# Performance work log

Hardware: AMD Instinct MI355X
Metric: run time of the kernel (lower is better)

The kernel has to match this reference:

```python
import jax, jax.numpy as jnp
import numpy as np

NUM_TIMESCALES = 16
MAX_TIME = 100.0
N_HEADS = 4
MLP_WIDTH = 128
HIDDEN_EACH = 128  # hidden_size // attn_n_heads = 512 // 4


def setup_inputs() -> dict:
    key = jax.random.key(0)
    ks = jax.random.split(key, 8)
    B, ROWS_PER_PAT, V = 32, 64, 32
    R = B * ROWS_PER_PAT
    # patient i has counts[i] observations, laid out row-major in its block of rows
    counts = 512 + 16 * np.arange(B)
    M = np.zeros((R, V), np.int32)
    for i in range(B):
        flat = M[i * ROWS_PER_PAT:(i + 1) * ROWS_PER_PAT].reshape(-1)
        flat[:counts[i]] = 1
    n_obs = int(counts.sum())        # 24320
    max_n_obs = int(counts.max())    # 1008
    n_in = 2 * NUM_TIMESCALES + 2    # 34

    def lin(k, o, i_):
        kw, kb = jax.random.split(k)
        return (jax.random.normal(kw, (o, i_)) * (1.0 / np.sqrt(i_)),
                jax.random.normal(kb, (o,)) * 0.01)

    W0, b0 = lin(ks[0], MLP_WIDTH, n_in)
    W1, b1 = lin(ks[1], MLP_WIDTH, MLP_WIDTH)
    W2, b2 = lin(ks[2], HIDDEN_EACH, MLP_WIDTH)
    Wq, bq = lin(ks[3], HIDDEN_EACH, HIDDEN_EACH)
    Wk, bk = lin(ks[4], HIDDEN_EACH, HIDDEN_EACH)
    return {
        "times": jax.random.uniform(ks[5], (R,)) * MAX_TIME,
        "time_ptr": jnp.arange(R + 1),
        "X": jax.random.normal(ks[6], (R, V)),
        "M": jnp.asarray(M),
        "obs_idx": jnp.repeat(jnp.arange(B), ROWS_PER_PAT),
        "pat_idx": jnp.arange(B),
        "W0": W0, "b0": b0, "W1": W1, "b1": b1, "W2": W2, "b2": b2,
        "Wq": Wq, "bq": bq, "Wk": Wk, "bk": bk,
        "n_obs": n_obs, "max_n_obs": max_n_obs,
    }


def reference(times, time_ptr, X, M, obs_idx, pat_idx,
              W0, b0, W1, b1, W2, b2, Wq, bq, Wk, bk, n_obs, max_n_obs):
    B = pat_idx.shape[0]
    # --- ragged scatter: (time_row, var) observations -> padded per-patient sets ---
    rows, cols = jnp.nonzero(M, size=n_obs)          # row-major, grouped by patient
    p = obs_idx[rows]                                # patient id per observation
    vals = X[rows, cols]
    t_arr = jnp.repeat(times, jnp.diff(time_ptr), total_repeat_length=X.shape[0])
    t = t_arr[rows]
    lens = jnp.bincount(p, length=B)
    starts = jnp.cumsum(lens) - lens
    pos = jnp.arange(n_obs) - starts[p]              # within-patient slot index
    Sv = jnp.zeros((B, max_n_obs), X.dtype).at[p, pos].set(cols.astype(X.dtype))
    Sx = jnp.zeros((B, max_n_obs), X.dtype).at[p, pos].set(vals)
    St = jnp.zeros((B, max_n_obs), X.dtype).at[p, pos].set(t)
    pad = jnp.arange(max_n_obs)[None, :] >= lens[:, None]   # True = padding
    # --- time embedding + feature concat: [sin, cos, var, value] ---
    timescales = MAX_TIME ** jnp.linspace(0.0, 1.0, NUM_TIMESCALES)
    st = St[..., None] / timescales
    new_X = jnp.concatenate([jnp.sin(st), jnp.cos(st), Sv[..., None], Sx[..., None]], axis=-1)
    # --- encoder MLP (depth 3 -> 1 hidden layer, eval mode: dropout is identity) ---
    h = jax.nn.relu(new_X @ W0.T + b0)
    h = jax.nn.relu(h @ W1.T + b1)
    enc = h @ W2.T + b2                              # [B, L, 128]
    # --- masked self-attention weights (only q/k matter; output is discarded) ---
    L = max_n_obs
    hd = HIDDEN_EACH // N_HEADS
    q = (enc @ Wq.T + bq).reshape(B, L, N_HEADS, hd)
    k = (enc @ Wk.T + bk).reshape(B, L, N_HEADS, hd)
    scores = jnp.einsum('blhd,bmhd->bhlm', q, k) / np.sqrt(hd)
    scores = jnp.where(pad[:, None, None, :], -1e30, scores)
    attn = jax.nn.softmax(scores, axis=-1)           # [B, H, L, L]
    w = attn[:, :, -1, :]                            # last-query attention row
    summed = jnp.einsum('bhl,ble->bhe', w, enc)      # [B, H, 128]
    return summed.reshape(B, -1)                     # [B, 512]
```

## Files before the change

### kernel.cpp

```cpp
#include <hip/hip_runtime.h>

#define B_PAT 32
#define RPP 64
#define RTOT 2048
#define NV 32
#define LMAX 1008
#define NTS 16
#define NIN 64
#define HW 128
#define LDSP 136
#define NCH 16
#define CH 63
#define ELD 132
#define RLD 136

typedef __attribute__((ext_vector_type(8))) short short8;
typedef __attribute__((ext_vector_type(4))) float floatx4;

__device__ __forceinline__ ushort f2b(float f) {
  unsigned int x = __float_as_uint(f);
  unsigned int r = (x + 0x7FFFu + ((x >> 16) & 1u)) >> 16;
  return (ushort)r;
}
__device__ __forceinline__ unsigned int pack2(ushort lo, ushort hi) {
  return (unsigned int)lo | ((unsigned int)hi << 16);
}
__device__ __forceinline__ unsigned long long shfl_up_u64(unsigned long long x, int off) {
  int lo = (int)(x & 0xffffffffull), hi = (int)(x >> 32);
  lo = __shfl_up(lo, off); hi = __shfl_up(hi, off);
  return ((unsigned long long)(unsigned int)hi << 32) | (unsigned long long)(unsigned int)lo;
}

__global__ __launch_bounds__(256) void k1_features(
    const float* __restrict__ times, const int* __restrict__ time_ptr,
    const float* __restrict__ X, const int* __restrict__ M,
    const int* __restrict__ obs_idx, const float* __restrict__ W0,
    const float* __restrict__ W1, const float* __restrict__ W2,
    ushort* __restrict__ feats, ushort* __restrict__ W0p,
    ushort* __restrict__ W1b, ushort* __restrict__ W2b, int* __restrict__ lens)
{
  const int b = blockIdx.x;
  const int t = threadIdx.x;
  if (b == B_PAT) {
    for (int i = t; i < HW * NIN; i += 256) {
      int n = i >> 6, k = i & 63;
      W0p[i] = (k < 34) ? f2b(W0[n * 34 + k]) : (ushort)0;
    }
    return;
  }
  if (b == B_PAT + 1) {
    for (int i = t; i < HW * HW; i += 256) W1b[i] = f2b(W1[i]);
    return;
  }
  if (b == B_PAT + 2) {
    for (int i = t; i < HW * HW; i += 256) W2b[i] = f2b(W2[i]);
    return;
  }
  __shared__ float inv_ts[NTS];
  __shared__ unsigned long long wsum[4];
  __shared__ int rowlist[RPP];
  __shared__ int rowpos[RPP];
  if (t < NTS) {
    float ts = powf(100.0f, (float)t * (1.0f / 15.0f));
    inv_ts[t] = 1.0f / ts;
  }
  const int lane = t & 63, wv = t >> 6;
  unsigned long long acc = 0ull;
  unsigned long long pref[8];
  const int rbase = t * 8;
#pragma unroll
  for (int j = 0; j < 8; ++j) {
    int r = rbase + j;
    int c = 0, pres = 0;
    if (obs_idx[r] == b) {
      pres = 1;
      const int4* mp = (const int4*)(M + r * NV);
#pragma unroll
      for (int q = 0; q < 8; ++q) {
        int4 m4 = mp[q];
        c += (m4.x != 0) + (m4.y != 0) + (m4.z != 0) + (m4.w != 0);
      }
    }
    pref[j] = acc;
    acc += (unsigned long long)(unsigned int)c | ((unsigned long long)pres << 32);
  }
  unsigned long long incl = acc;
  for (int off = 1; off < 64; off <<= 1) {
    unsigned long long v = shfl_up_u64(incl, off);
    if (lane >= off) incl += v;
  }
  if (lane == 63) wsum[wv] = incl;
  __syncthreads();
  unsigned long long wbase = 0ull;
  for (int w = 0; w < wv; ++w) wbase += wsum[w];
  unsigned long long totalall = wsum[0] + wsum[1] + wsum[2] + wsum[3];
  const int total = (int)(totalall & 0xffffffffull);
  const int nrows = (int)(totalall >> 32);
  unsigned long long myexcl = wbase + incl - acc;
#pragma unroll
  for (int j = 0; j < 8; ++j) {
    int r = rbase + j;
    if (obs_idx[r] == b) {
      unsigned long long p = myexcl + pref[j];
      int ord = (int)(p >> 32);
      if (ord < RPP) { rowlist[ord] = r; rowpos[ord] = (int)(p & 0xffffffffull); }
    }
  }
  if (t == 0) lens[b] = total;
  __syncthreads();
  const int o = t >> 2, sub = t & 3;
  if (o < nrows && o < RPP) {
    int r = rowlist[o];
    int base = rowpos[o];
    int lo = 0, hi = RTOT - 1;
    while (lo < hi) { int mid = (lo + hi + 1) >> 1; if (time_ptr[mid] <= r) lo = mid; else hi = mid - 1; }
    float tv = times[lo];
    float sv[NTS], cv[NTS];
#pragma unroll
    for (int i = 0; i < NTS; ++i) {
      float a = tv * inv_ts[i];
      sv[i] = sinf(a); cv[i] = cosf(a);
    }
    int cnt = 0;
    const int cb = sub * 8;
    for (int vv = 0; vv < cb; ++vv) cnt += (M[r * NV + vv] != 0);
    int pos = base + cnt;
    for (int vv = cb; vv < cb + 8; ++vv) {
      if (M[r * NV + vv] != 0) {
        unsigned int* fp = (unsigned int*)(feats + ((size_t)b * LMAX + pos) * NIN);
#pragma unroll
        for (int i = 0; i < 8; ++i) fp[i] = pack2(f2b(sv[2 * i]), f2b(sv[2 * i + 1]));
#pragma unroll
        for (int i = 0; i < 8; ++i) fp[8 + i] = pack2(f2b(cv[2 * i]), f2b(cv[2 * i + 1]));
        fp[16] = pack2(f2b((float)vv), f2b(X[r * NV + vv]));
#pragma unroll
        for (int i = 17; i < 32; ++i) fp[i] = 0u;
        ++pos;
      }
    }
  }
  {
    uint4 z = make_uint4(0u, 0u, 0u, 0u);
    uint4 one; one.x = one.y = one.z = one.w = 0x3F803F80u;
    for (int pos = total + t; pos < LMAX; pos += 256) {
      uint4* fp = (uint4*)(feats + ((size_t)b * LMAX + pos) * NIN);
      fp[0] = z; fp[1] = z; fp[2] = one; fp[3] = one;
      fp[4] = z; fp[5] = z; fp[6] = z; fp[7] = z;
    }
  }
}

__global__ __launch_bounds__(256) void k2_mlp(
    const ushort* __restrict__ feats, const ushort* __restrict__ W0p,
    const float* __restrict__ b0, const ushort* __restrict__ W1b,
    const float* __restrict__ b1, const ushort* __restrict__ W2b,
    const float* __restrict__ b2, float* __restrict__ enc)
{
  __shared__ ushort bufA[64 * LDSP];
  __shared__ ushort bufB[64 * LDSP];
  const int tid = threadIdx.x;
  const int wv = tid >> 6, lane = tid & 63;
  const int m16 = lane & 15, quad = lane >> 4;
  const int rowl = wv * 16 + m16;
  const size_t grow = (size_t)blockIdx.x * 64;
  {
    const short8* ar = (const short8*)(feats + (grow + rowl) * NIN);
    short8 a0 = ar[quad];
    short8 a1 = ar[4 + quad];
#pragma unroll
    for (int nt = 0; nt < 8; ++nt) {
      int n = nt * 16 + m16;
      const short8* br = (const short8*)(W0p + n * NIN);
      floatx4 acc = {0.f, 0.f, 0.f, 0.f};
      acc = __builtin_amdgcn_mfma_f32_16x16x32_bf16(a0, br[quad], acc, 0, 0, 0);
      acc = __builtin_amdgcn_mfma_f32_16x16x32_bf16(a1, br[4 + quad], acc, 0, 0, 0);
      float bias = b0[n];
#pragma unroll
      for (int i = 0; i < 4; ++i) {
        float vv = fmaxf(acc[i] + bias, 0.0f);
        bufA[(wv * 16 + quad * 4 + i) * LDSP + n] = f2b(vv);
      }
    }
  }
  __syncthreads();
  {
#pragma unroll
    for (int nt = 0; nt < 8; ++nt) {
      int n = nt * 16 + m16;
      floatx4 acc = {0.f, 0.f, 0.f, 0.f};
#pragma unroll
      for (int ks = 0; ks < 4; ++ks) {
        short8 a = *(const short8*)(bufA + rowl * LDSP + ks * 32 + quad * 8);
        short8 bb = *(const short8*)(W1b + n * HW + ks * 32 + quad * 8);
        acc = __builtin_amdgcn_mfma_f32_16x16x32_bf16(a, bb, acc, 0, 0, 0);
      }
      float bias = b1[n];
#pragma unroll
      for (int i = 0; i < 4; ++i) {
        float vv = fmaxf(acc[i] + bias, 0.0f);
        bufB[(wv * 16 + quad * 4 + i) * LDSP + n] = f2b(vv);
      }
    }
  }
  __syncthreads();
  {
#pragma unroll
    for (int nt = 0; nt < 8; ++nt) {
      int n = nt * 16 + m16;
      floatx4 acc = {0.f, 0.f, 0.f, 0.f};
#pragma unroll
      for (int ks = 0; ks < 4; ++ks) {
        short8 a = *(const short8*)(bufB + rowl * LDSP + ks * 32 + quad * 8);
        short8 bb = *(const short8*)(W2b + n * HW + ks * 32 + quad * 8);
        acc = __builtin_amdgcn_mfma_f32_16x16x32_bf16(a, bb, acc, 0, 0, 0);
      }
      float bias = b2[n];
#pragma unroll
      for (int i = 0; i < 4; ++i) {
        enc[(grow + wv * 16 + quad * 4 + i) * HW + n] = acc[i] + bias;
      }
    }
  }
}

__global__ __launch_bounds__(256) void k3_qr(
    const float* __restrict__ enc, const float* __restrict__ Wq,
    const float* __restrict__ bq, const float* __restrict__ Wk,
    float* __restrict__ r_all)
{
  const int b = blockIdx.x;
  const int tid = threadIdx.x;
  __shared__ float encq_s[HW], q_s[HW];
  const float* encb = enc + (size_t)b * LMAX * HW;
  if (tid < HW) encq_s[tid] = encb[(LMAX - 1) * HW + tid];
  __syncthreads();
  if (tid < HW) {
    float acc = bq[tid];
    const float4* wr = (const float4*)(Wq + tid * HW);
#pragma unroll 8
    for (int e4 = 0; e4 < 32; ++e4) {
      float4 w4 = wr[e4];
      acc += w4.x * encq_s[e4 * 4 + 0] + w4.y * encq_s[e4 * 4 + 1] +
             w4.z * encq_s[e4 * 4 + 2] + w4.w * encq_s[e4 * 4 + 3];
    }
    q_s[tid] = acc;
  }
  __syncthreads();
  const float scale = 0.17677669529663687f;
  for (int idx = tid; idx < 512; idx += 256) {
    int h = idx >> 7, e = idx & 127;
    float acc = 0.f;
#pragma unroll 8
    for (int d = 0; d < 32; ++d) acc += Wk[(h * 32 + d) * HW + e] * q_s[h * 32 + d];
    r_all[b * 512 + idx] = acc * scale;
  }
}

__global__ __launch_bounds__(256) void k3_chunk(
    const float* __restrict__ enc, const int* __restrict__ lens,
    const float* __restrict__ r_all, float* __restrict__ partial,
    float2* __restrict__ mxsm)
{
  const int bx = blockIdx.x;
  const int b = bx >> 4, c = bx & 15;
  const int tid = threadIdx.x;
  const int len = lens[b];
  const int start = c * CH;
  int valid = len - start; if (valid > CH) valid = CH;
  if (valid <= 0) {
    if (tid < 4) mxsm[bx * 4 + tid] = make_float2(-1e30f, 0.0f);
    return;
  }
  __shared__ float encs[CH * ELD];
  __shared__ float r_s[4 * RLD];
  __shared__ float lg[4 * 64];
  __shared__ float mx_s[4], sm_s[4];
  const float* encb = enc + ((size_t)b * LMAX + start) * HW;
  for (int i = tid; i < valid * 32; i += 256) {
    int row = i >> 5, e4 = i & 31;
    float4 v = ((const float4*)(encb + row * HW))[e4];
    *(float4*)(&encs[row * ELD + e4 * 4]) = v;
  }
  for (int i = tid; i < 512; i += 256)
    r_s[(i >> 7) * RLD + (i & 127)] = r_all[b * 512 + i];
  __syncthreads();
  {
    int m = tid >> 2, h = tid & 3;
    if (m < valid) {
      const float4* ev = (const float4*)(&encs[m * ELD]);
      const float4* rv = (const float4*)(&r_s[h * RLD]);
      float acc = 0.f;
#pragma unroll
      for (int e4 = 0; e4 < 32; ++e4) {
        float4 v = ev[e4], r = rv[e4];
        acc += v.x * r.x + v.y * r.y + v.z * r.z + v.w * r.w;
      }
      lg[h * 64 + m] = acc;
    }
  }
  __syncthreads();
  {
    const int wv = tid >> 6, lane = tid & 63;
    float v = (lane < valid) ? lg[wv * 64 + lane] : -1e30f;
    float mx = v;
#pragma unroll
    for (int o = 32; o >= 1; o >>= 1) mx = fmaxf(mx, __shfl_xor(mx, o));
    float p = (lane < valid) ? expf(v - mx) : 0.f;
    lg[wv * 64 + lane] = p;
    float sm = p;
#pragma unroll
    for (int o = 32; o >= 1; o >>= 1) sm += __shfl_xor(sm, o);
    if (lane == 0) { mx_s[wv] = mx; sm_s[wv] = sm; }
  }
  __syncthreads();
  for (int idx = tid; idx < 512; idx += 256) {
    int h = idx >> 7, e = idx & 127;
    float acc = 0.f;
    for (int m = 0; m < valid; ++m)
      acc += lg[h * 64 + m] * encs[m * ELD + e];
    partial[(size_t)bx * 512 + idx] = acc;
  }
  if (tid < 4) mxsm[bx * 4 + tid] = make_float2(mx_s[tid], sm_s[tid]);
}

__global__ __launch_bounds__(256) void k4_combine(
    const float* __restrict__ partial, const float2* __restrict__ mxsm,
    float* __restrict__ out)
{
  const int b = blockIdx.x;
  const int tid = threadIdx.x;
  __shared__ float f_s[NCH * 4];
  if (tid < 4) {
    int h = tid;
    float2 v[NCH];
    float M = -1e30f;
#pragma unroll
    for (int c = 0; c < NCH; ++c) {
      v[c] = mxsm[(b * NCH + c) * 4 + h];
      if (v[c].y > 0.f) M = fmaxf(M, v[c].x);
    }
    float S = 0.f;
#pragma unroll
    for (int c = 0; c < NCH; ++c)
      if (v[c].y > 0.f) S += v[c].y * expf(v[c].x - M);
    float invS = 1.0f / S;
#pragma unroll
    for (int c = 0; c < NCH; ++c)
      f_s[c * 4 + h] = (v[c].y > 0.f) ? expf(v[c].x - M) * invS : 0.f;
  }
  __syncthreads();
  for (int idx = tid; idx < 512; idx += 256) {
    int h = idx >> 7;
    float acc = 0.f;
#pragma unroll
    for (int c = 0; c < NCH; ++c)
      acc += partial[((size_t)(b * NCH + c)) * 512 + idx] * f_s[c * 4 + h];
    out[b * 512 + idx] = acc;
  }
}

extern "C" void kernel_launch(void* const* d_in, const int* in_sizes, int n_in,
                              void* d_out, int out_size, void* d_ws, size_t ws_size,
                              hipStream_t stream) {
  const float* times = (const float*)d_in[0];
  const int* time_ptr = (const int*)d_in[1];
  const float* X = (const float*)d_in[2];
  const int* M = (const int*)d_in[3];
  const int* obs_idx = (const int*)d_in[4];
  const float* W0 = (const float*)d_in[6];
  const float* b0 = (const float*)d_in[7];
  const float* W1 = (const float*)d_in[8];
  const float* b1 = (const float*)d_in[9];
  const float* W2 = (const float*)d_in[10];
  const float* b2 = (const float*)d_in[11];
  const float* Wq = (const float*)d_in[12];
  const float* bq = (const float*)d_in[13];
  const float* Wk = (const float*)d_in[14];
  float* out = (float*)d_out;

  char* ws = (char*)d_ws;
  size_t off = 0;
  ushort* feats = (ushort*)(ws + off); off += (size_t)B_PAT * LMAX * NIN * sizeof(ushort);
  ushort* W0p = (ushort*)(ws + off); off += (size_t)HW * NIN * sizeof(ushort);
  ushort* W1b = (ushort*)(ws + off); off += (size_t)HW * HW * sizeof(ushort);
  ushort* W2b = (ushort*)(ws + off); off += (size_t)HW * HW * sizeof(ushort);
  off = (off + 255) & ~(size_t)255;
  int* lens = (int*)(ws + off); off += 256;
  float* enc = (float*)(ws + off); off += (size_t)B_PAT * LMAX * HW * sizeof(float);
  float* r_all = (float*)(ws + off); off += (size_t)B_PAT * 512 * sizeof(float);
  float* partial = (float*)(ws + off); off += (size_t)B_PAT * NCH * 512 * sizeof(float);
  float2* mxsm = (float2*)(ws + off); off += (size_t)B_PAT * NCH * 4 * sizeof(float2);

  k1_features<<<B_PAT + 3, 256, 0, stream>>>(times, time_ptr, X, M, obs_idx,
                                             W0, W1, W2, feats, W0p, W1b, W2b, lens);
  k2_mlp<<<(B_PAT * LMAX) / 64, 256, 0, stream>>>(feats, W0p, b0, W1b, b1, W2b, b2, enc);
  k3_qr<<<B_PAT, 256, 0, stream>>>(enc, Wq, bq, Wk, r_all);
  k3_chunk<<<B_PAT * NCH, 256, 0, stream>>>(enc, lens, r_all, partial, mxsm);
  k4_combine<<<B_PAT, 256, 0, stream>>>(partial, mxsm, out);
}
```

Before: 157.7 us.

## Fuse encoder MLP into attention chunk kernel and compute query in feature kernel

Runs the three-layer encoder MLP inside the per-chunk attention kernel and keeps each chunk's encodings in shared memory, so the full fp32 enc tensor is never written to or read back from global memory. The last-row query projection is computed separately in the feature kernel with a scalar fp32 MLP, which removes the separate query kernel and one launch. Chunks past a patient's length now skip the MLP work entirely. In exchange the fused kernel uses much more shared memory per block, which can lower occupancy, and the serial query path adds latency to the feature kernel.

```diff
diff --git a/kernel.cpp b/kernel.cpp
--- a/kernel.cpp
+++ b/kernel.cpp
@@ -17,6 +17,9 @@
 typedef __attribute__((ext_vector_type(8))) short short8;
 typedef __attribute__((ext_vector_type(4))) float floatx4;
 
+__device__ __forceinline__ float b2f(ushort u) {
+  union { float f; unsigned int i; } v; v.i = ((unsigned int)u) << 16; return v.f;
+}
 __device__ __forceinline__ ushort f2b(float f) {
   unsigned int x = __float_as_uint(f);
   unsigned int r = (x + 0x7FFFu + ((x >> 16) & 1u)) >> 16;
@@ -35,9 +38,13 @@
     const float* __restrict__ times, const int* __restrict__ time_ptr,
     const float* __restrict__ X, const int* __restrict__ M,
     const int* __restrict__ obs_idx, const float* __restrict__ W0,
-    const float* __restrict__ W1, const float* __restrict__ W2,
+    const float* __restrict__ b0, const float* __restrict__ W1,
+    const float* __restrict__ b1, const float* __restrict__ W2,
+    const float* __restrict__ b2, const float* __restrict__ Wq,
+    const float* __restrict__ bq, const float* __restrict__ Wk,
     ushort* __restrict__ feats, ushort* __restrict__ W0p,
-    ushort* __restrict__ W1b, ushort* __restrict__ W2b, int* __restrict__ lens)
+    ushort* __restrict__ W1b, ushort* __restrict__ W2b,
+    int* __restrict__ lens, float* __restrict__ r_all)
 {
   const int b = blockIdx.x;
   const int t = threadIdx.x;
@@ -148,116 +155,67 @@
       fp[4] = z; fp[5] = z; fp[6] = z; fp[7] = z;
     }
   }
-}
-
-__global__ __launch_bounds__(256) void k2_mlp(
+  __syncthreads();
+  __shared__ float x_s[64];
+  __shared__ float h0_s[HW], h1_s[HW], eq_s[HW], q_s[HW];
+  __shared__ float part[256];
+  if (t < 64) x_s[t] = b2f(feats[((size_t)b * LMAX + (LMAX - 1)) * NIN + t]);
+  __syncthreads();
+  if (t < HW) {
+    float a2 = b0[t];
+#pragma unroll 2
+    for (int k = 0; k < 34; ++k) a2 += W0[t * 34 + k] * x_s[k];
+    h0_s[t] = fmaxf(a2, 0.0f);
+  }
+  __syncthreads();
+  {
+    int oo = t & 127, hf = t >> 7;
+    float a2 = 0.f;
+    const float* wr = W1 + oo * HW + hf * 64;
+#pragma unroll 8
+    for (int k = 0; k < 64; ++k) a2 += wr[k] * h0_s[hf * 64 + k];
+    part[t] = a2;
+  }
+  __syncthreads();
+  if (t < HW) h1_s[t] = fmaxf(part[t] + part[t + 128] + b1[t], 0.0f);
+  __syncthreads();
+  {
+    int oo = t & 127, hf = t >> 7;
+    float a2 = 0.f;
+    const float* wr = W2 + oo * HW + hf * 64;
+#pragma unroll 8
+    for (int k = 0; k < 64; ++k) a2 += wr[k] * h1_s[hf * 64 + k];
+    part[t] = a2;
+  }
+  __syncthreads();
+  if (t < HW) eq_s[t] = part[t] + part[t + 128] + b2[t];
+  __syncthreads();
+  {
+    int oo = t & 127, hf = t >> 7;
+    float a2 = 0.f;
+    const float* wr = Wq + oo * HW + hf * 64;
+#pragma unroll 8
+    for (int k = 0; k < 64; ++k) a2 += wr[k] * eq_s[hf * 64 + k];
+    part[t] = a2;
+  }
+  __syncthreads();
+  if (t < HW) q_s[t] = part[t] + part[t + 128] + bq[t];
+  __syncthreads();
+  const float scale = 0.17677669529663687f;
+  for (int idx = t; idx < 512; idx += 256) {
+    int h = idx >> 7, e = idx & 127;
+    float a2 = 0.f;
+#pragma unroll 8
+    for (int d = 0; d < 32; ++d) a2 += Wk[(h * 32 + d) * HW + e] * q_s[h * 32 + d];
+    r_all[b * 512 + idx] = a2 * scale;
+  }
+}
+
+__global__ __launch_bounds__(256) void k2_fused(
     const ushort* __restrict__ feats, const ushort* __restrict__ W0p,
     const float* __restrict__ b0, const ushort* __restrict__ W1b,
     const float* __restrict__ b1, const ushort* __restrict__ W2b,
-    const float* __restrict__ b2, float* __restrict__ enc)
-{
-  __shared__ ushort bufA[64 * LDSP];
-  __shared__ ushort bufB[64 * LDSP];
-  const int tid = threadIdx.x;
-  const int wv = tid >> 6, lane = tid & 63;
-  const int m16 = lane & 15, quad = lane >> 4;
-  const int rowl = wv * 16 + m16;
-  const size_t grow = (size_t)blockIdx.x * 64;
-  {
-    const short8* ar = (const short8*)(feats + (grow + rowl) * NIN);
-    short8 a0 = ar[quad];
-    short8 a1 = ar[4 + quad];
-#pragma unroll
-    for (int nt = 0; nt < 8; ++nt) {
-      int n = nt * 16 + m16;
-      const short8* br = (const short8*)(W0p + n * NIN);
-      floatx4 acc = {0.f, 0.f, 0.f, 0.f};
-      acc = __builtin_amdgcn_mfma_f32_16x16x32_bf16(a0, br[quad], acc, 0, 0, 0);
-      acc = __builtin_amdgcn_mfma_f32_16x16x32_bf16(a1, br[4 + quad], acc, 0, 0, 0);
-      float bias = b0[n];
-#pragma unroll
-      for (int i = 0; i < 4; ++i) {
-        float vv = fmaxf(acc[i] + bias, 0.0f);
-        bufA[(wv * 16 + quad * 4 + i) * LDSP + n] = f2b(vv);
-      }
-    }
-  }
-  __syncthreads();
-  {
-#pragma unroll
-    for (int nt = 0; nt < 8; ++nt) {
-      int n = nt * 16 + m16;
-      floatx4 acc = {0.f, 0.f, 0.f, 0.f};
-#pragma unroll
-      for (int ks = 0; ks < 4; ++ks) {
-        short8 a = *(const short8*)(bufA + rowl * LDSP + ks * 32 + quad * 8);
-        short8 bb = *(const short8*)(W1b + n * HW + ks * 32 + quad * 8);
-        acc = __builtin_amdgcn_mfma_f32_16x16x32_bf16(a, bb, acc, 0, 0, 0);
-      }
-      float bias = b1[n];
-#pragma unroll
-      for (int i = 0; i < 4; ++i) {
-        float vv = fmaxf(acc[i] + bias, 0.0f);
-        bufB[(wv * 16 + quad * 4 + i) * LDSP + n] = f2b(vv);
-      }
-    }
-  }
-  __syncthreads();
-  {
-#pragma unroll
-    for (int nt = 0; nt < 8; ++nt) {
-      int n = nt * 16 + m16;
-      floatx4 acc = {0.f, 0.f, 0.f, 0.f};
-#pragma unroll
-      for (int ks = 0; ks < 4; ++ks) {
-        short8 a = *(const short8*)(bufB + rowl * LDSP + ks * 32 + quad * 8);
-        short8 bb = *(const short8*)(W2b + n * HW + ks * 32 + quad * 8);
-        acc = __builtin_amdgcn_mfma_f32_16x16x32_bf16(a, bb, acc, 0, 0, 0);
-      }
-      float bias = b2[n];
-#pragma unroll
-      for (int i = 0; i < 4; ++i) {
-        enc[(grow + wv * 16 + quad * 4 + i) * HW + n] = acc[i] + bias;
-      }
-    }
-  }
-}
-
-__global__ __launch_bounds__(256) void k3_qr(
-    const float* __restrict__ enc, const float* __restrict__ Wq,
-    const float* __restrict__ bq, const float* __restrict__ Wk,
-    float* __restrict__ r_all)
-{
-  const int b = blockIdx.x;
-  const int tid = threadIdx.x;
-  __shared__ float encq_s[HW], q_s[HW];
-  const float* encb = enc + (size_t)b * LMAX * HW;
-  if (tid < HW) encq_s[tid] = encb[(LMAX - 1) * HW + tid];
-  __syncthreads();
-  if (tid < HW) {
-    float acc = bq[tid];
-    const float4* wr = (const float4*)(Wq + tid * HW);
-#pragma unroll 8
-    for (int e4 = 0; e4 < 32; ++e4) {
-      float4 w4 = wr[e4];
-      acc += w4.x * encq_s[e4 * 4 + 0] + w4.y * encq_s[e4 * 4 + 1] +
-             w4.z * encq_s[e4 * 4 + 2] + w4.w * encq_s[e4 * 4 + 3];
-    }
-    q_s[tid] = acc;
-  }
-  __syncthreads();
-  const float scale = 0.17677669529663687f;
-  for (int idx = tid; idx < 512; idx += 256) {
-    int h = idx >> 7, e = idx & 127;
-    float acc = 0.f;
-#pragma unroll 8
-    for (int d = 0; d < 32; ++d) acc += Wk[(h * 32 + d) * HW + e] * q_s[h * 32 + d];
-    r_all[b * 512 + idx] = acc * scale;
-  }
-}
-
-__global__ __launch_bounds__(256) void k3_chunk(
-    const float* __restrict__ enc, const int* __restrict__ lens,
+    const float* __restrict__ b2, const int* __restrict__ lens,
     const float* __restrict__ r_all, float* __restrict__ partial,
     float2* __restrict__ mxsm)
 {
@@ -269,38 +227,98 @@
   int valid = len - start; if (valid > CH) valid = CH;
   if (valid <= 0) {
     if (tid < 4) mxsm[bx * 4 + tid] = make_float2(-1e30f, 0.0f);
+    for (int i = tid; i < 512; i += 256) partial[(size_t)bx * 512 + i] = 0.f;
     return;
   }
+  __shared__ ushort bufA[64 * LDSP];
+  __shared__ ushort bufB[64 * LDSP];
   __shared__ float encs[CH * ELD];
   __shared__ float r_s[4 * RLD];
   __shared__ float lg[4 * 64];
   __shared__ float mx_s[4], sm_s[4];
-  const float* encb = enc + ((size_t)b * LMAX + start) * HW;
-  for (int i = tid; i < valid * 32; i += 256) {
-    int row = i >> 5, e4 = i & 31;
-    float4 v = ((const float4*)(encb + row * HW))[e4];
-    *(float4*)(&encs[row * ELD + e4 * 4]) = v;
-  }
+  const int wv = tid >> 6, lane = tid & 63;
+  const int m16 = lane & 15, quad = lane >> 4;
+  const int rowl = wv * 16 + m16;
+  const size_t fbase = (size_t)b * LMAX + start;
   for (int i = tid; i < 512; i += 256)
     r_s[(i >> 7) * RLD + (i & 127)] = r_all[b * 512 + i];
+  {
+    const int arow = (rowl < CH) ? rowl : (CH - 1);
+    const short8* ar = (const short8*)(feats + (fbase + arow) * NIN);
+    short8 a0 = ar[quad];
+    short8 a1 = ar[4 + quad];
+#pragma unroll
+    for (int nt = 0; nt < 8; ++nt) {
+      int n = nt * 16 + m16;
+      const short8* br = (const short8*)(W0p + n * NIN);
+      floatx4 acc2 = {0.f, 0.f, 0.f, 0.f};
+      acc2 = __builtin_amdgcn_mfma_f32_16x16x32_bf16(a0, br[quad], acc2, 0, 0, 0);
+      acc2 = __builtin_amdgcn_mfma_f32_16x16x32_bf16(a1, br[4 + quad], acc2, 0, 0, 0);
+      float bias = b0[n];
+#pragma unroll
+      for (int i = 0; i < 4; ++i) {
+        float vv = fmaxf(acc2[i] + bias, 0.0f);
+        bufA[(wv * 16 + quad * 4 + i) * LDSP + n] = f2b(vv);
+      }
+    }
+  }
+  __syncthreads();
+  {
+#pragma unroll
+    for (int nt = 0; nt < 8; ++nt) {
+      int n = nt * 16 + m16;
+      floatx4 acc2 = {0.f, 0.f, 0.f, 0.f};
+#pragma unroll
+      for (int ks = 0; ks < 4; ++ks) {
+        short8 a = *(const short8*)(bufA + rowl * LDSP + ks * 32 + quad * 8);
+        short8 bb = *(const short8*)(W1b + n * HW + ks * 32 + quad * 8);
+        acc2 = __builtin_amdgcn_mfma_f32_16x16x32_bf16(a, bb, acc2, 0, 0, 0);
+      }
+      float bias = b1[n];
+#pragma unroll
+      for (int i = 0; i < 4; ++i) {
+        float vv = fmaxf(acc2[i] + bias, 0.0f);
+        bufB[(wv * 16 + quad * 4 + i) * LDSP + n] = f2b(vv);
+      }
+    }
+  }
+  __syncthreads();
+  {
+#pragma unroll
+    for (int nt = 0; nt < 8; ++nt) {
+      int n = nt * 16 + m16;
+      floatx4 acc2 = {0.f, 0.f, 0.f, 0.f};
+#pragma unroll
+      for (int ks = 0; ks < 4; ++ks) {
+        short8 a = *(const short8*)(bufB + rowl * LDSP + ks * 32 + quad * 8);
+        short8 bb = *(const short8*)(W2b + n * HW + ks * 32 + quad * 8);
+        acc2 = __builtin_amdgcn_mfma_f32_16x16x32_bf16(a, bb, acc2, 0, 0, 0);
+      }
+      float bias = b2[n];
+#pragma unroll
+      for (int i = 0; i < 4; ++i) {
+        int orow = wv * 16 + quad * 4 + i;
+        if (orow < CH) encs[orow * ELD + n] = acc2[i] + bias;
+      }
+    }
+  }
   __syncthreads();
   {
     int m = tid >> 2, h = tid & 3;
     if (m < valid) {
       const float4* ev = (const float4*)(&encs[m * ELD]);
       const float4* rv = (const float4*)(&r_s[h * RLD]);
-      float acc = 0.f;
+      float acc2 = 0.f;
 #pragma unroll
       for (int e4 = 0; e4 < 32; ++e4) {
         float4 v = ev[e4], r = rv[e4];
-        acc += v.x * r.x + v.y * r.y + v.z * r.z + v.w * r.w;
-      }
-      lg[h * 64 + m] = acc;
-    }
-  }
-  __syncthreads();
-  {
-    const int wv = tid >> 6, lane = tid & 63;
+        acc2 += v.x * r.x + v.y * r.y + v.z * r.z + v.w * r.w;
+      }
+      lg[h * 64 + m] = acc2;
+    }
+  }
+  __syncthreads();
+  {
     float v = (lane < valid) ? lg[wv * 64 + lane] : -1e30f;
     float mx = v;
 #pragma unroll
@@ -315,10 +333,10 @@
   __syncthreads();
   for (int idx = tid; idx < 512; idx += 256) {
     int h = idx >> 7, e = idx & 127;
-    float acc = 0.f;
+    float acc2 = 0.f;
     for (int m = 0; m < valid; ++m)
-      acc += lg[h * 64 + m] * encs[m * ELD + e];
-    partial[(size_t)bx * 512 + idx] = acc;
+      acc2 += lg[h * 64 + m] * encs[m * ELD + e];
+    partial[(size_t)bx * 512 + idx] = acc2;
   }
   if (tid < 4) mxsm[bx * 4 + tid] = make_float2(mx_s[tid], sm_s[tid]);
 }
@@ -386,15 +404,14 @@
   ushort* W2b = (ushort*)(ws + off); off += (size_t)HW * HW * sizeof(ushort);
   off = (off + 255) & ~(size_t)255;
   int* lens = (int*)(ws + off); off += 256;
-  float* enc = (float*)(ws + off); off += (size_t)B_PAT * LMAX * HW * sizeof(float);
   float* r_all = (float*)(ws + off); off += (size_t)B_PAT * 512 * sizeof(float);
   float* partial = (float*)(ws + off); off += (size_t)B_PAT * NCH * 512 * sizeof(float);
   float2* mxsm = (float2*)(ws + off); off += (size_t)B_PAT * NCH * 4 * sizeof(float2);
 
   k1_features<<<B_PAT + 3, 256, 0, stream>>>(times, time_ptr, X, M, obs_idx,
-                                             W0, W1, W2, feats, W0p, W1b, W2b, lens);
-  k2_mlp<<<(B_PAT * LMAX) / 64, 256, 0, stream>>>(feats, W0p, b0, W1b, b1, W2b, b2, enc);
-  k3_qr<<<B_PAT, 256, 0, stream>>>(enc, Wq, bq, Wk, r_all);
-  k3_chunk<<<B_PAT * NCH, 256, 0, stream>>>(enc, lens, r_all, partial, mxsm);
+                                             W0, b0, W1, b1, W2, b2, Wq, bq, Wk,
+                                             feats, W0p, W1b, W2b, lens, r_all);
+  k2_fused<<<B_PAT * NCH, 256, 0, stream>>>(feats, W0p, b0, W1b, b1, W2b, b2,
+                                            lens, r_all, partial, mxsm);
   k4_combine<<<B_PAT, 256, 0, stream>>>(partial, mxsm, out);
 }
```

Result: faster. 151.9 us (-3.7%).

## Fuse feature build, MLP encoder and attention chunks into one per-row-pair kernel

Applied to the files above, without the earlier changes.

Restructures the pipeline so that each block takes two time rows of a patient, builds their feature tiles in LDS, runs the MLP with MFMA and immediately computes attention partials. The padded per-patient feature buffer and the full fp32 enc tensor in global memory are gone, and padding rows are no longer run through the MLP. The last-query row is recomputed separately in fp32 in a small kernel that produces q and r_all. This removes the large global round trips and the wasted padded work, at the cost of more kernels, more LDS per block and twice as many partial chunks to combine.

```diff
diff --git a/kernel.cpp b/kernel.cpp
--- a/kernel.cpp
+++ b/kernel.cpp
@@ -1,16 +1,15 @@
 #include <hip/hip_runtime.h>
 
 #define B_PAT 32
-#define RPP 64
 #define RTOT 2048
 #define NV 32
 #define LMAX 1008
 #define NTS 16
 #define NIN 64
+#define TLD 72
 #define HW 128
 #define LDSP 136
-#define NCH 16
-#define CH 63
+#define NCH2 32
 #define ELD 132
 #define RLD 136
 
@@ -25,146 +24,273 @@
 __device__ __forceinline__ unsigned int pack2(ushort lo, ushort hi) {
   return (unsigned int)lo | ((unsigned int)hi << 16);
 }
-__device__ __forceinline__ unsigned long long shfl_up_u64(unsigned long long x, int off) {
-  int lo = (int)(x & 0xffffffffull), hi = (int)(x >> 32);
-  lo = __shfl_up(lo, off); hi = __shfl_up(hi, off);
-  return ((unsigned long long)(unsigned int)hi << 32) | (unsigned long long)(unsigned int)lo;
-}
-
-__global__ __launch_bounds__(256) void k1_features(
+__device__ __forceinline__ float tscale(int i) {
+  return exp2f((float)i * (6.643856189774724f / 15.0f));
+}
+
+__global__ __launch_bounds__(256) void kA(
     const float* __restrict__ times, const int* __restrict__ time_ptr,
-    const float* __restrict__ X, const int* __restrict__ M,
-    const int* __restrict__ obs_idx, const float* __restrict__ W0,
+    const int* __restrict__ M, const float* __restrict__ W0,
     const float* __restrict__ W1, const float* __restrict__ W2,
-    ushort* __restrict__ feats, ushort* __restrict__ W0p,
-    ushort* __restrict__ W1b, ushort* __restrict__ W2b, int* __restrict__ lens)
+    int* __restrict__ row_cnt, float* __restrict__ trow,
+    ushort* __restrict__ W0p, ushort* __restrict__ W1b, ushort* __restrict__ W2b)
+{
+  const int blk = blockIdx.x, t = threadIdx.x;
+  if (blk >= 8) {
+    if (blk == 8) {
+      for (int i = t; i < HW * NIN; i += 256) {
+        int n = i >> 6, k = i & 63;
+        W0p[i] = (k < 34) ? f2b(W0[n * 34 + k]) : (ushort)0;
+      }
+    } else if (blk == 9) {
+      for (int i = t; i < HW * HW; i += 256) W1b[i] = f2b(W1[i]);
+    } else {
+      for (int i = t; i < HW * HW; i += 256) W2b[i] = f2b(W2[i]);
+    }
+    return;
+  }
+  const int r = blk * 256 + t;
+  const int4* mp = (const int4*)(M + r * NV);
+  int c = 0;
+#pragma unroll
+  for (int q = 0; q < 8; ++q) {
+    int4 m4 = mp[q];
+    c += (m4.x != 0) + (m4.y != 0) + (m4.z != 0) + (m4.w != 0);
+  }
+  row_cnt[r] = c;
+  int lo = 0, hi = RTOT - 1;
+  while (lo < hi) { int mid = (lo + hi + 1) >> 1; if (time_ptr[mid] <= r) lo = mid; else hi = mid - 1; }
+  trow[r] = times[lo];
+}
+
+__global__ __launch_bounds__(256) void kB(
+    const int* __restrict__ obs_idx, const int* __restrict__ row_cnt,
+    int* __restrict__ base, int* __restrict__ rowstart, int* __restrict__ lens)
+{
+  const int t = threadIdx.x;
+  const int lane = t & 63, wv = t >> 6;
+  __shared__ int wsum[4];
+  __shared__ int gpre[RTOT + 1];
+  __shared__ int rowstart_s[B_PAT + 1];
+  int cnt[8], pref[8];
+  int a = 0;
+  const int rbase = t * 8;
+#pragma unroll
+  for (int j = 0; j < 8; ++j) {
+    cnt[j] = row_cnt[rbase + j];
+    pref[j] = a; a += cnt[j];
+  }
+  int incl = a;
+  for (int off = 1; off < 64; off <<= 1) {
+    int v = __shfl_up(incl, off);
+    if (lane >= off) incl += v;
+  }
+  if (lane == 63) wsum[wv] = incl;
+  if (t == 0) rowstart_s[B_PAT] = RTOT;
+  __syncthreads();
+  int wbase = 0;
+  for (int w = 0; w < wv; ++w) wbase += wsum[w];
+  int excl = wbase + incl - a;
+#pragma unroll
+  for (int j = 0; j < 8; ++j) gpre[rbase + j] = excl + pref[j];
+  if (t == 255) gpre[RTOT] = excl + a;
+  for (int r = t; r < RTOT; r += 256) {
+    int b = obs_idx[r];
+    if (r == 0 || obs_idx[r - 1] != b) rowstart_s[b] = r;
+  }
+  __syncthreads();
+  if (t < B_PAT) {
+    int rs = rowstart_s[t], re = rowstart_s[t + 1];
+    lens[t] = gpre[re] - gpre[rs];
+    rowstart[t] = rs;
+  }
+  if (t == 0) rowstart[B_PAT] = RTOT;
+  for (int r = t; r < RTOT; r += 256)
+    base[r] = gpre[r] - gpre[rowstart_s[obs_idx[r]]];
+}
+
+__global__ __launch_bounds__(256) void kC(
+    const int* __restrict__ M, const float* __restrict__ X,
+    const float* __restrict__ trow, const int* __restrict__ base,
+    const int* __restrict__ row_cnt, const int* __restrict__ rowstart,
+    const int* __restrict__ lens,
+    const float* __restrict__ W0, const float* __restrict__ b0,
+    const float* __restrict__ W1, const float* __restrict__ b1,
+    const float* __restrict__ W2, const float* __restrict__ b2,
+    const float* __restrict__ Wq, const float* __restrict__ bq,
+    const float* __restrict__ Wk, float* __restrict__ r_all)
 {
   const int b = blockIdx.x;
   const int t = threadIdx.x;
-  if (b == B_PAT) {
-    for (int i = t; i < HW * NIN; i += 256) {
-      int n = i >> 6, k = i & 63;
-      W0p[i] = (k < 34) ? f2b(W0[n * 34 + k]) : (ushort)0;
-    }
+  __shared__ float x_s[64];
+  __shared__ float h0[HW], h1[HW], eq[HW], q_s[HW], part[256];
+  __shared__ int rc_s[2];
+  if (t < 64) x_s[t] = 0.0f;
+  if (t == 0) {
+    const int pos = LMAX - 1;
+    if (pos < lens[b]) {
+      int r = rowstart[b];
+      while (base[r] + row_cnt[r] <= pos) ++r;
+      int k = pos - base[r], c = 0;
+      for (int cc = 0; cc < NV; ++cc)
+        if (M[r * NV + cc] != 0) { if (k == 0) { c = cc; break; } --k; }
+      rc_s[0] = r; rc_s[1] = c;
+    } else rc_s[0] = -1;
+  }
+  __syncthreads();
+  if (rc_s[0] < 0) {
+    if (t >= 16 && t < 32) x_s[t] = 1.0f;
+  } else {
+    int r = rc_s[0], c = rc_s[1];
+    if (t < 16) {
+      float a = trow[r] / tscale(t);
+      x_s[t] = sinf(a); x_s[16 + t] = cosf(a);
+    }
+    if (t == 0) { x_s[32] = (float)c; x_s[33] = X[r * NV + c]; }
+  }
+  __syncthreads();
+  if (t < HW) {
+    float a = b0[t];
+#pragma unroll 2
+    for (int k = 0; k < 34; ++k) a += W0[t * 34 + k] * x_s[k];
+    h0[t] = fmaxf(a, 0.0f);
+  }
+  __syncthreads();
+  {
+    int oo = t & 127, hf = t >> 7;
+    float a = 0.f;
+    const float* wr = W1 + oo * HW + hf * 64;
+#pragma unroll 8
+    for (int k = 0; k < 64; ++k) a += wr[k] * h0[hf * 64 + k];
+    part[t] = a;
+  }
+  __syncthreads();
+  if (t < HW) h1[t] = fmaxf(part[t] + part[t + 128] + b1[t], 0.0f);
+  __syncthreads();
+  {
+    int oo = t & 127, hf = t >> 7;
+    float a = 0.f;
+    const float* wr = W2 + oo * HW + hf * 64;
+#pragma unroll 8
+    for (int k = 0; k < 64; ++k) a += wr[k] * h1[hf * 64 + k];
+    part[t] = a;
+  }
+  __syncthreads();
+  if (t < HW) eq[t] = part[t] + part[t + 128] + b2[t];
+  __syncthreads();
+  {
+    int oo = t & 127, hf = t >> 7;
+    float a = 0.f;
+    const float* wr = Wq + oo * HW + hf * 64;
+#pragma unroll 8
+    for (int k = 0; k < 64; ++k) a += wr[k] * eq[hf * 64 + k];
+    part[t] = a;
+  }
+  __syncthreads();
+  if (t < HW) q_s[t] = part[t] + part[t + 128] + bq[t];
+  __syncthreads();
+  const float scale = 0.17677669529663687f;
+  for (int idx = t; idx < 512; idx += 256) {
+    int h = idx >> 7, e = idx & 127;
+    float a = 0.f;
+#pragma unroll 8
+    for (int d = 0; d < 32; ++d) a += Wk[(h * 32 + d) * HW + e] * q_s[h * 32 + d];
+    r_all[b * 512 + idx] = a * scale;
+  }
+}
+
+__global__ __launch_bounds__(256) void kD(
+    const int* __restrict__ M, const float* __restrict__ X,
+    const float* __restrict__ trow, const int* __restrict__ base,
+    const int* __restrict__ row_cnt, const int* __restrict__ rowstart,
+    const ushort* __restrict__ W0p, const float* __restrict__ b0,
+    const ushort* __restrict__ W1b, const float* __restrict__ b1,
+    const ushort* __restrict__ W2b, const float* __restrict__ b2,
+    const float* __restrict__ r_all, float* __restrict__ partial,
+    float2* __restrict__ mxsm)
+{
+  const int bx = blockIdx.x;
+  const int b = bx >> 5, j = bx & 31;
+  const int t = threadIdx.x;
+  const int wv = t >> 6, lane = t & 63;
+  const int rs = rowstart[b], re = rowstart[b + 1];
+  const int r0 = rs + 2 * j;
+  if (r0 >= re) {
+    if (t < 4) mxsm[bx * 4 + t] = make_float2(-1e30f, 0.0f);
     return;
   }
-  if (b == B_PAT + 1) {
-    for (int i = t; i < HW * HW; i += 256) W1b[i] = f2b(W1[i]);
+  const int r1 = r0 + 1;
+  const bool has1 = (r1 < re);
+  const int pstart = base[r0];
+  const int valid = row_cnt[r0] + (has1 ? row_cnt[r1] : 0);
+  if (valid <= 0) {
+    if (t < 4) mxsm[bx * 4 + t] = make_float2(-1e30f, 0.0f);
     return;
   }
-  if (b == B_PAT + 2) {
-    for (int i = t; i < HW * HW; i += 256) W2b[i] = f2b(W2[i]);
-    return;
-  }
-  __shared__ float inv_ts[NTS];
-  __shared__ unsigned long long wsum[4];
-  __shared__ int rowlist[RPP];
-  __shared__ int rowpos[RPP];
-  if (t < NTS) {
-    float ts = powf(100.0f, (float)t * (1.0f / 15.0f));
-    inv_ts[t] = 1.0f / ts;
-  }
-  const int lane = t & 63, wv = t >> 6;
-  unsigned long long acc = 0ull;
-  unsigned long long pref[8];
-  const int rbase = t * 8;
-#pragma unroll
-  for (int j = 0; j < 8; ++j) {
-    int r = rbase + j;
-    int c = 0, pres = 0;
-    if (obs_idx[r] == b) {
-      pres = 1;
-      const int4* mp = (const int4*)(M + r * NV);
-#pragma unroll
-      for (int q = 0; q < 8; ++q) {
-        int4 m4 = mp[q];
-        c += (m4.x != 0) + (m4.y != 0) + (m4.z != 0) + (m4.w != 0);
-      }
-    }
-    pref[j] = acc;
-    acc += (unsigned long long)(unsigned int)c | ((unsigned long long)pres << 32);
-  }
-  unsigned long long incl = acc;
-  for (int off = 1; off < 64; off <<= 1) {
-    unsigned long long v = shfl_up_u64(incl, off);
-    if (lane >= off) incl += v;
-  }
-  if (lane == 63) wsum[wv] = incl;
-  __syncthreads();
-  unsigned long long wbase = 0ull;
-  for (int w = 0; w < wv; ++w) wbase += wsum[w];
-  unsigned long long totalall = wsum[0] + wsum[1] + wsum[2] + wsum[3];
-  const int total = (int)(totalall & 0xffffffffull);
-  const int nrows = (int)(totalall >> 32);
-  unsigned long long myexcl = wbase + incl - acc;
-#pragma unroll
-  for (int j = 0; j < 8; ++j) {
-    int r = rbase + j;
-    if (obs_idx[r] == b) {
-      unsigned long long p = myexcl + pref[j];
-      int ord = (int)(p >> 32);
-      if (ord < RPP) { rowlist[ord] = r; rowpos[ord] = (int)(p & 0xffffffffull); }
-    }
-  }
-  if (t == 0) lens[b] = total;
-  __syncthreads();
-  const int o = t >> 2, sub = t & 3;
-  if (o < nrows && o < RPP) {
-    int r = rowlist[o];
-    int base = rowpos[o];
-    int lo = 0, hi = RTOT - 1;
-    while (lo < hi) { int mid = (lo + hi + 1) >> 1; if (time_ptr[mid] <= r) lo = mid; else hi = mid - 1; }
-    float tv = times[lo];
-    float sv[NTS], cv[NTS];
-#pragma unroll
-    for (int i = 0; i < NTS; ++i) {
-      float a = tv * inv_ts[i];
-      sv[i] = sinf(a); cv[i] = cosf(a);
-    }
-    int cnt = 0;
-    const int cb = sub * 8;
-    for (int vv = 0; vv < cb; ++vv) cnt += (M[r * NV + vv] != 0);
-    int pos = base + cnt;
-    for (int vv = cb; vv < cb + 8; ++vv) {
-      if (M[r * NV + vv] != 0) {
-        unsigned int* fp = (unsigned int*)(feats + ((size_t)b * LMAX + pos) * NIN);
-#pragma unroll
-        for (int i = 0; i < 8; ++i) fp[i] = pack2(f2b(sv[2 * i]), f2b(sv[2 * i + 1]));
-#pragma unroll
-        for (int i = 0; i < 8; ++i) fp[8 + i] = pack2(f2b(cv[2 * i]), f2b(cv[2 * i + 1]));
-        fp[16] = pack2(f2b((float)vv), f2b(X[r * NV + vv]));
-#pragma unroll
-        for (int i = 17; i < 32; ++i) fp[i] = 0u;
-        ++pos;
-      }
-    }
-  }
+  __shared__ __align__(16) char arena[55296];
+  ushort* tile = (ushort*)(arena);
+  ushort* bufA = (ushort*)(arena + 9216);
+  float*  encs = (float*)(arena);
+  ushort* bufB = (ushort*)(arena + 33792);
+  float*  r_s  = (float*)(arena + 51200);
+  float*  lg   = (float*)(arena + 53376);
+  unsigned int* mapP = (unsigned int*)(arena + 54400);
+  unsigned int* mapT = (unsigned int*)(arena + 54656);
+  ushort* tps  = (ushort*)(arena + 54912);
+  float*  mx_s = (float*)(arena + 55040);
+  float*  sm_s = (float*)(arena + 55056);
   {
     uint4 z = make_uint4(0u, 0u, 0u, 0u);
-    uint4 one; one.x = one.y = one.z = one.w = 0x3F803F80u;
-    for (int pos = total + t; pos < LMAX; pos += 256) {
-      uint4* fp = (uint4*)(feats + ((size_t)b * LMAX + pos) * NIN);
-      fp[0] = z; fp[1] = z; fp[2] = one; fp[3] = one;
-      fp[4] = z; fp[5] = z; fp[6] = z; fp[7] = z;
-    }
-  }
-}
-
-__global__ __launch_bounds__(256) void k2_mlp(
-    const ushort* __restrict__ feats, const ushort* __restrict__ W0p,
-    const float* __restrict__ b0, const ushort* __restrict__ W1b,
-    const float* __restrict__ b1, const ushort* __restrict__ W2b,
-    const float* __restrict__ b2, float* __restrict__ enc)
-{
-  __shared__ ushort bufA[64 * LDSP];
-  __shared__ ushort bufB[64 * LDSP];
-  const int tid = threadIdx.x;
-  const int wv = tid >> 6, lane = tid & 63;
+    uint4* tp = (uint4*)tile;
+    for (int i = t; i < 576; i += 256) tp[i] = z;
+    for (int i = t; i < 512; i += 256)
+      r_s[(i >> 7) * RLD + (i & 127)] = r_all[b * 512 + i];
+  }
+  __syncthreads();
+  if (wv == 0) {
+    int rr = lane >> 5, cc = lane & 31;
+    int r = r0 + rr;
+    bool present = (rr == 0 || has1) ? (M[r * NV + cc] != 0) : false;
+    unsigned long long mask = __ballot(present);
+    unsigned int mh = (rr == 0) ? (unsigned int)mask : (unsigned int)(mask >> 32);
+    if (present) {
+      int rank = __popc(mh & ((1u << cc) - 1u));
+      int lp = base[r] - pstart + rank;
+      mapP[lp] = pack2(f2b((float)cc), f2b(X[r * NV + cc]));
+      mapT[lp] = (unsigned int)rr;
+    }
+  }
+  if (wv == 1 && lane < 32) {
+    int rr = lane >> 4, i = lane & 15;
+    if (rr == 0 || has1) {
+      float a = trow[r0 + rr] / tscale(i);
+      tps[rr * 32 + i] = f2b(sinf(a));
+      tps[rr * 32 + 16 + i] = f2b(cosf(a));
+    }
+  }
+  __syncthreads();
+  {
+    int lp = t >> 2, jj = t & 3;
+    if (lp < valid) {
+      int rr = (int)mapT[lp];
+      unsigned int* dst = (unsigned int*)(tile + lp * TLD);
+      const unsigned int* tp = ((const unsigned int*)tps) + rr * 16;
+      if (jj == 0) {
+#pragma unroll
+        for (int k = 0; k < 8; ++k) dst[k] = tp[k];
+      } else if (jj == 1) {
+#pragma unroll
+        for (int k = 0; k < 8; ++k) dst[8 + k] = tp[8 + k];
+      } else if (jj == 2) {
+        dst[16] = mapP[lp];
+      }
+    }
+  }
+  __syncthreads();
   const int m16 = lane & 15, quad = lane >> 4;
   const int rowl = wv * 16 + m16;
-  const size_t grow = (size_t)blockIdx.x * 64;
-  {
-    const short8* ar = (const short8*)(feats + (grow + rowl) * NIN);
+  {
+    const short8* ar = (const short8*)(tile + rowl * TLD);
     short8 a0 = ar[quad];
     short8 a1 = ar[4 + quad];
 #pragma unroll
@@ -216,76 +342,13 @@
       }
       float bias = b2[n];
 #pragma unroll
-      for (int i = 0; i < 4; ++i) {
-        enc[(grow + wv * 16 + quad * 4 + i) * HW + n] = acc[i] + bias;
-      }
-    }
-  }
-}
-
-__global__ __launch_bounds__(256) void k3_qr(
-    const float* __restrict__ enc, const float* __restrict__ Wq,
-    const float* __restrict__ bq, const float* __restrict__ Wk,
-    float* __restrict__ r_all)
-{
-  const int b = blockIdx.x;
-  const int tid = threadIdx.x;
-  __shared__ float encq_s[HW], q_s[HW];
-  const float* encb = enc + (size_t)b * LMAX * HW;
-  if (tid < HW) encq_s[tid] = encb[(LMAX - 1) * HW + tid];
-  __syncthreads();
-  if (tid < HW) {
-    float acc = bq[tid];
-    const float4* wr = (const float4*)(Wq + tid * HW);
-#pragma unroll 8
-    for (int e4 = 0; e4 < 32; ++e4) {
-      float4 w4 = wr[e4];
-      acc += w4.x * encq_s[e4 * 4 + 0] + w4.y * encq_s[e4 * 4 + 1] +
-             w4.z * encq_s[e4 * 4 + 2] + w4.w * encq_s[e4 * 4 + 3];
-    }
-    q_s[tid] = acc;
-  }
-  __syncthreads();
-  const float scale = 0.17677669529663687f;
-  for (int idx = tid; idx < 512; idx += 256) {
-    int h = idx >> 7, e = idx & 127;
-    float acc = 0.f;
-#pragma unroll 8
-    for (int d = 0; d < 32; ++d) acc += Wk[(h * 32 + d) * HW + e] * q_s[h * 32 + d];
-    r_all[b * 512 + idx] = acc * scale;
-  }
-}
-
-__global__ __launch_bounds__(256) void k3_chunk(
-    const float* __restrict__ enc, const int* __restrict__ lens,
-    const float* __restrict__ r_all, float* __restrict__ partial,
-    float2* __restrict__ mxsm)
-{
-  const int bx = blockIdx.x;
-  const int b = bx >> 4, c = bx & 15;
-  const int tid = threadIdx.x;
-  const int len = lens[b];
-  const int start = c * CH;
-  int valid = len - start; if (valid > CH) valid = CH;
-  if (valid <= 0) {
-    if (tid < 4) mxsm[bx * 4 + tid] = make_float2(-1e30f, 0.0f);
-    return;
-  }
-  __shared__ float encs[CH * ELD];
-  __shared__ float r_s[4 * RLD];
-  __shared__ float lg[4 * 64];
-  __shared__ float mx_s[4], sm_s[4];
-  const float* encb = enc + ((size_t)b * LMAX + start) * HW;
-  for (int i = tid; i < valid * 32; i += 256) {
-    int row = i >> 5, e4 = i & 31;
-    float4 v = ((const float4*)(encb + row * HW))[e4];
-    *(float4*)(&encs[row * ELD + e4 * 4]) = v;
-  }
-  for (int i = tid; i < 512; i += 256)
-    r_s[(i >> 7) * RLD + (i & 127)] = r_all[b * 512 + i];
-  __syncthreads();
-  {
-    int m = tid >> 2, h = tid & 3;
+      for (int i = 0; i < 4; ++i)
+        encs[(wv * 16 + quad * 4 + i) * ELD + n] = acc[i] + bias;
+    }
+  }
+  __syncthreads();
+  {
+    int m = t >> 2, h = t & 3;
     if (m < valid) {
       const float4* ev = (const float4*)(&encs[m * ELD]);
       const float4* rv = (const float4*)(&r_s[h * RLD]);
@@ -300,7 +363,6 @@
   }
   __syncthreads();
   {
-    const int wv = tid >> 6, lane = tid & 63;
     float v = (lane < valid) ? lg[wv * 64 + lane] : -1e30f;
     float mx = v;
 #pragma unroll
@@ -313,14 +375,14 @@
     if (lane == 0) { mx_s[wv] = mx; sm_s[wv] = sm; }
   }
   __syncthreads();
-  for (int idx = tid; idx < 512; idx += 256) {
+  for (int idx = t; idx < 512; idx += 256) {
     int h = idx >> 7, e = idx & 127;
     float acc = 0.f;
     for (int m = 0; m < valid; ++m)
       acc += lg[h * 64 + m] * encs[m * ELD + e];
     partial[(size_t)bx * 512 + idx] = acc;
   }
-  if (tid < 4) mxsm[bx * 4 + tid] = make_float2(mx_s[tid], sm_s[tid]);
+  if (t < 4) mxsm[bx * 4 + t] = make_float2(mx_s[t], sm_s[t]);
 }
 
 __global__ __launch_bounds__(256) void k4_combine(
@@ -329,23 +391,23 @@
 {
   const int b = blockIdx.x;
   const int tid = threadIdx.x;
-  __shared__ float f_s[NCH * 4];
+  __shared__ float f_s[NCH2 * 4];
   if (tid < 4) {
     int h = tid;
-    float2 v[NCH];
+    float2 v[NCH2];
     float M = -1e30f;
 #pragma unroll
-    for (int c = 0; c < NCH; ++c) {
-      v[c] = mxsm[(b * NCH + c) * 4 + h];
+    for (int c = 0; c < NCH2; ++c) {
+      v[c] = mxsm[(b * NCH2 + c) * 4 + h];
       if (v[c].y > 0.f) M = fmaxf(M, v[c].x);
     }
     float S = 0.f;
 #pragma unroll
-    for (int c = 0; c < NCH; ++c)
+    for (int c = 0; c < NCH2; ++c)
       if (v[c].y > 0.f) S += v[c].y * expf(v[c].x - M);
     float invS = 1.0f / S;
 #pragma unroll
-    for (int c = 0; c < NCH; ++c)
+    for (int c = 0; c < NCH2; ++c)
       f_s[c * 4 + h] = (v[c].y > 0.f) ? expf(v[c].x - M) * invS : 0.f;
   }
   __syncthreads();
@@ -353,8 +415,8 @@
     int h = idx >> 7;
     float acc = 0.f;
 #pragma unroll
-    for (int c = 0; c < NCH; ++c)
-      acc += partial[((size_t)(b * NCH + c)) * 512 + idx] * f_s[c * 4 + h];
+    for (int c = 0; c < NCH2; ++c)
+      acc += partial[((size_t)(b * NCH2 + c)) * 512 + idx] * f_s[c * 4 + h];
     out[b * 512 + idx] = acc;
   }
 }
@@ -380,21 +442,23 @@
 
   char* ws = (char*)d_ws;
   size_t off = 0;
-  ushort* feats = (ushort*)(ws + off); off += (size_t)B_PAT * LMAX * NIN * sizeof(ushort);
-  ushort* W0p = (ushort*)(ws + off); off += (size_t)HW * NIN * sizeof(ushort);
-  ushort* W1b = (ushort*)(ws + off); off += (size_t)HW * HW * sizeof(ushort);
-  ushort* W2b = (ushort*)(ws + off); off += (size_t)HW * HW * sizeof(ushort);
-  off = (off + 255) & ~(size_t)255;
+  int* row_cnt = (int*)(ws + off); off += RTOT * 4;
+  float* trow = (float*)(ws + off); off += RTOT * 4;
+  int* base = (int*)(ws + off); off += RTOT * 4;
+  int* rowstart = (int*)(ws + off); off += 256;
   int* lens = (int*)(ws + off); off += 256;
-  float* enc = (float*)(ws + off); off += (size_t)B_PAT * LMAX * HW * sizeof(float);
-  float* r_all = (float*)(ws + off); off += (size_t)B_PAT * 512 * sizeof(float);
-  float* partial = (float*)(ws + off); off += (size_t)B_PAT * NCH * 512 * sizeof(float);
-  float2* mxsm = (float2*)(ws + off); off += (size_t)B_PAT * NCH * 4 * sizeof(float2);
-
-  k1_features<<<B_PAT + 3, 256, 0, stream>>>(times, time_ptr, X, M, obs_idx,
-                                             W0, W1, W2, feats, W0p, W1b, W2b, lens);
-  k2_mlp<<<(B_PAT * LMAX) / 64, 256, 0, stream>>>(feats, W0p, b0, W1b, b1, W2b, b2, enc);
-  k3_qr<<<B_PAT, 256, 0, stream>>>(enc, Wq, bq, Wk, r_all);
-  k3_chunk<<<B_PAT * NCH, 256, 0, stream>>>(enc, lens, r_all, partial, mxsm);
+  ushort* W0p = (ushort*)(ws + off); off += (size_t)HW * NIN * 2;
+  ushort* W1b = (ushort*)(ws + off); off += (size_t)HW * HW * 2;
+  ushort* W2b = (ushort*)(ws + off); off += (size_t)HW * HW * 2;
+  float* r_all = (float*)(ws + off); off += (size_t)B_PAT * 512 * 4;
+  float* partial = (float*)(ws + off); off += (size_t)B_PAT * NCH2 * 512 * 4;
+  float2* mxsm = (float2*)(ws + off); off += (size_t)B_PAT * NCH2 * 4 * 8;
+
+  kA<<<11, 256, 0, stream>>>(times, time_ptr, M, W0, W1, W2, row_cnt, trow, W0p, W1b, W2b);
+  kB<<<1, 256, 0, stream>>>(obs_idx, row_cnt, base, rowstart, lens);
+  kC<<<B_PAT, 256, 0, stream>>>(M, X, trow, base, row_cnt, rowstart, lens,
+                                W0, b0, W1, b1, W2, b2, Wq, bq, Wk, r_all);
+  kD<<<B_PAT * NCH2, 256, 0, stream>>>(M, X, trow, base, row_cnt, rowstart,
+                                       W0p, b0, W1b, b1, W2b, b2, r_all, partial, mxsm);
   k4_combine<<<B_PAT, 256, 0, stream>>>(partial, mxsm, out);
 }
```

Result: slower. 167.2 us (+6.1%).
